# Performance work log

Measured on AMD Instinct MI355X. Metric: run time of the kernel, lower is better.

The kernel has to match this reference:

```python
import jax, jax.numpy as jnp
import numpy as np

N_NODES = 50000
N_EDGES = 800000
D_IN = 128
D_OUT = 64


def setup_inputs() -> dict:
    key = jax.random.key(0)
    k_x, k_src, k_dst, k_val, k_w = jax.random.split(key, 5)
    x = jax.random.normal(k_x, (N_NODES, D_IN), dtype=jnp.float32)
    edge_src = jax.random.randint(k_src, (N_EDGES,), 0, N_NODES, dtype=jnp.int32)
    edge_dst = jnp.sort(jax.random.randint(k_dst, (N_EDGES,), 0, N_NODES, dtype=jnp.int32))
    edge_vals = jax.random.uniform(k_val, (N_EDGES,), dtype=jnp.float32)
    # Xavier-uniform init for weight, zeros for bias (matches reset_parameters)
    limit = float(np.sqrt(6.0 / (D_IN + D_OUT)))
    weight = jax.random.uniform(k_w, (D_IN, D_OUT), minval=-limit, maxval=limit, dtype=jnp.float32)
    bias = jnp.zeros((D_OUT,), dtype=jnp.float32)
    return {"x": x, "edge_src": edge_src, "edge_dst": edge_dst,
            "edge_vals": edge_vals, "weight": weight, "bias": bias}


def reference(x, edge_src, edge_dst, edge_vals, weight, bias):
    # Dense projection: [N, D_in] @ [D_in, D_out] -> [N, D_out]
    h = x @ weight
    # Sparse adjacency matmul (torch.spmm): out[i] = sum_{(j->i) in E} A_val * h[j]
    msgs = edge_vals[:, None] * h[edge_src]          # [E, D_out]
    agg = jax.ops.segment_sum(msgs, edge_dst, num_segments=N_NODES)  # [N, D_out]
    return agg + bias
```

## Files before the change

### kernel.cpp

```cpp
#include <hip/hip_runtime.h>

#define D_IN  128
#define D_OUT 64

typedef float    nfloat4 __attribute__((ext_vector_type(4)));
typedef _Float16 half4_t __attribute__((ext_vector_type(4)));

__global__ __launch_bounds__(256, 4) void gemm_rowptr_kernel(
    const float* __restrict__ x, const float* __restrict__ w,
    _Float16* __restrict__ h, int n_nodes,
    const int* __restrict__ dst, int* __restrict__ row_ptr, int n_edges,
    int gemm_blocks)
{
    __shared__ float Xs[64 * 132];
    __shared__ float Ws[128 * 64];

    if ((int)blockIdx.x >= gemm_blocks) {
        int rb   = (int)blockIdx.x - gemm_blocks;
        int base = rb * 1024 + (int)threadIdx.x;
        #pragma unroll
        for (int j = 0; j < 4; ++j) {
            int e = base + j * 256;
            if (e < n_edges) {
                int d1 = dst[e];
                int d0 = (e == 0) ? -1 : dst[e - 1];
                for (int q = d0 + 1; q <= d1; ++q) row_ptr[q] = e;
                if (e == n_edges - 1) {
                    for (int q = d1 + 1; q <= n_nodes; ++q) row_ptr[q] = n_edges;
                }
            }
        }
        return;
    }

    const int t   = threadIdx.x;
    const int tx  = t & 15;
    const int ty  = t >> 4;
    const int node0 = blockIdx.x * 64;

    #pragma unroll
    for (int j = 0; j < 8; ++j) {
        int idx = j * 256 + t;
        int k   = idx >> 4;
        int c   = idx & 15;
        float4 v = *(const float4*)&w[k * D_OUT + c * 4];
        *(float4*)&Ws[k * 64 + c * 4] = v;
    }
    #pragma unroll
    for (int j = 0; j < 8; ++j) {
        int idx = j * 256 + t;
        int r   = idx >> 5;
        int c   = idx & 31;
        int gn  = node0 + r;
        float4 v = make_float4(0.f, 0.f, 0.f, 0.f);
        if (gn < n_nodes) v = *(const float4*)&x[(size_t)gn * D_IN + c * 4];
        *(float4*)&Xs[r * 132 + c * 4] = v;
    }
    __syncthreads();

    float4 acc[4];
    #pragma unroll
    for (int i = 0; i < 4; ++i) acc[i] = make_float4(0.f, 0.f, 0.f, 0.f);

    const int d0 = tx * 4;
    const int n0 = ty * 4;

    #pragma unroll 2
    for (int k = 0; k < D_IN; k += 4) {
        float4 xa[4], wb[4];
        #pragma unroll
        for (int i = 0; i < 4; ++i)
            xa[i] = *(const float4*)&Xs[(n0 + i) * 132 + k];
        #pragma unroll
        for (int r = 0; r < 4; ++r)
            wb[r] = *(const float4*)&Ws[(k + r) * 64 + d0];
        #pragma unroll
        for (int i = 0; i < 4; ++i) {
            acc[i].x = fmaf(xa[i].x, wb[0].x, acc[i].x);
            acc[i].y = fmaf(xa[i].x, wb[0].y, acc[i].y);
            acc[i].z = fmaf(xa[i].x, wb[0].z, acc[i].z);
            acc[i].w = fmaf(xa[i].x, wb[0].w, acc[i].w);
            acc[i].x = fmaf(xa[i].y, wb[1].x, acc[i].x);
            acc[i].y = fmaf(xa[i].y, wb[1].y, acc[i].y);
            acc[i].z = fmaf(xa[i].y, wb[1].z, acc[i].z);
            acc[i].w = fmaf(xa[i].y, wb[1].w, acc[i].w);
            acc[i].x = fmaf(xa[i].z, wb[2].x, acc[i].x);
            acc[i].y = fmaf(xa[i].z, wb[2].y, acc[i].y);
            acc[i].z = fmaf(xa[i].z, wb[2].z, acc[i].z);
            acc[i].w = fmaf(xa[i].z, wb[2].w, acc[i].w);
            acc[i].x = fmaf(xa[i].w, wb[3].x, acc[i].x);
            acc[i].y = fmaf(xa[i].w, wb[3].y, acc[i].y);
            acc[i].z = fmaf(xa[i].w, wb[3].z, acc[i].z);
            acc[i].w = fmaf(xa[i].w, wb[3].w, acc[i].w);
        }
    }

    #pragma unroll
    for (int i = 0; i < 4; ++i) {
        int gn = node0 + n0 + i;
        if (gn < n_nodes) {
            half4_t hv;
            hv.x = (_Float16)acc[i].x;
            hv.y = (_Float16)acc[i].y;
            hv.z = (_Float16)acc[i].z;
            hv.w = (_Float16)acc[i].w;
            *(half4_t*)&h[(size_t)gn * D_OUT + d0] = hv;
        }
    }
}

__global__ __launch_bounds__(256) void aggregate_kernel(
    const half4_t* __restrict__ h4, const int* __restrict__ src,
    const float* __restrict__ vals, const int* __restrict__ row_ptr,
    const float* __restrict__ bias, float* __restrict__ out, int n_nodes)
{
    int wave = (blockIdx.x * blockDim.x + threadIdx.x) >> 6;
    int lane = threadIdx.x & 63;
    if (wave >= n_nodes) return;
    int sub = lane >> 4;
    int d4  = lane & 15;

    int b = row_ptr[wave];
    int e = row_ptr[wave + 1];

    float4 bb = *(const float4*)&bias[d4 * 4];

    float4 acc0 = make_float4(0.f, 0.f, 0.f, 0.f);
    float4 acc1 = make_float4(0.f, 0.f, 0.f, 0.f);

    int k = b + sub;
    for (; k + 12 < e; k += 16) {
        int   s0 = __builtin_nontemporal_load(&src[k]);
        int   s1 = __builtin_nontemporal_load(&src[k + 4]);
        int   s2 = __builtin_nontemporal_load(&src[k + 8]);
        int   s3 = __builtin_nontemporal_load(&src[k + 12]);
        float v0 = __builtin_nontemporal_load(&vals[k]);
        float v1 = __builtin_nontemporal_load(&vals[k + 4]);
        float v2 = __builtin_nontemporal_load(&vals[k + 8]);
        float v3 = __builtin_nontemporal_load(&vals[k + 12]);
        half4_t h0 = h4[(size_t)s0 * 16 + d4];
        half4_t h1 = h4[(size_t)s1 * 16 + d4];
        half4_t h2 = h4[(size_t)s2 * 16 + d4];
        half4_t h3 = h4[(size_t)s3 * 16 + d4];
        acc0.x = fmaf(v0, (float)h0.x, acc0.x);
        acc0.y = fmaf(v0, (float)h0.y, acc0.y);
        acc0.z = fmaf(v0, (float)h0.z, acc0.z);
        acc0.w = fmaf(v0, (float)h0.w, acc0.w);
        acc1.x = fmaf(v1, (float)h1.x, acc1.x);
        acc1.y = fmaf(v1, (float)h1.y, acc1.y);
        acc1.z = fmaf(v1, (float)h1.z, acc1.z);
        acc1.w = fmaf(v1, (float)h1.w, acc1.w);
        acc0.x = fmaf(v2, (float)h2.x, acc0.x);
        acc0.y = fmaf(v2, (float)h2.y, acc0.y);
        acc0.z = fmaf(v2, (float)h2.z, acc0.z);
        acc0.w = fmaf(v2, (float)h2.w, acc0.w);
        acc1.x = fmaf(v3, (float)h3.x, acc1.x);
        acc1.y = fmaf(v3, (float)h3.y, acc1.y);
        acc1.z = fmaf(v3, (float)h3.z, acc1.z);
        acc1.w = fmaf(v3, (float)h3.w, acc1.w);
    }
    for (; k + 4 < e; k += 8) {
        int   s0 = __builtin_nontemporal_load(&src[k]);
        int   s1 = __builtin_nontemporal_load(&src[k + 4]);
        float v0 = __builtin_nontemporal_load(&vals[k]);
        float v1 = __builtin_nontemporal_load(&vals[k + 4]);
        half4_t h0 = h4[(size_t)s0 * 16 + d4];
        half4_t h1 = h4[(size_t)s1 * 16 + d4];
        acc0.x = fmaf(v0, (float)h0.x, acc0.x);
        acc0.y = fmaf(v0, (float)h0.y, acc0.y);
        acc0.z = fmaf(v0, (float)h0.z, acc0.z);
        acc0.w = fmaf(v0, (float)h0.w, acc0.w);
        acc1.x = fmaf(v1, (float)h1.x, acc1.x);
        acc1.y = fmaf(v1, (float)h1.y, acc1.y);
        acc1.z = fmaf(v1, (float)h1.z, acc1.z);
        acc1.w = fmaf(v1, (float)h1.w, acc1.w);
    }
    if (k < e) {
        int   s0 = src[k];
        float v0 = vals[k];
        half4_t h0 = h4[(size_t)s0 * 16 + d4];
        acc0.x = fmaf(v0, (float)h0.x, acc0.x);
        acc0.y = fmaf(v0, (float)h0.y, acc0.y);
        acc0.z = fmaf(v0, (float)h0.z, acc0.z);
        acc0.w = fmaf(v0, (float)h0.w, acc0.w);
    }

    float4 acc;
    acc.x = acc0.x + acc1.x;
    acc.y = acc0.y + acc1.y;
    acc.z = acc0.z + acc1.z;
    acc.w = acc0.w + acc1.w;

    #pragma unroll
    for (int off = 16; off < 64; off <<= 1) {
        acc.x += __shfl_xor(acc.x, off, 64);
        acc.y += __shfl_xor(acc.y, off, 64);
        acc.z += __shfl_xor(acc.z, off, 64);
        acc.w += __shfl_xor(acc.w, off, 64);
    }

    if (sub == 0) {
        nfloat4 o;
        o.x = acc.x + bb.x;
        o.y = acc.y + bb.y;
        o.z = acc.z + bb.z;
        o.w = acc.w + bb.w;
        __builtin_nontemporal_store(o, (nfloat4*)&out[(size_t)wave * D_OUT + d4 * 4]);
    }
}

extern "C" void kernel_launch(void* const* d_in, const int* in_sizes, int n_in,
                              void* d_out, int out_size, void* d_ws, size_t ws_size,
                              hipStream_t stream)
{
    const float* x         = (const float*)d_in[0];
    const int*   edge_src  = (const int*)  d_in[1];
    const int*   edge_dst  = (const int*)  d_in[2];
    const float* edge_vals = (const float*)d_in[3];
    const float* weight    = (const float*)d_in[4];
    const float* bias      = (const float*)d_in[5];
    float*       out       = (float*)d_out;

    const int n_nodes = in_sizes[0] / D_IN;
    const int n_edges = in_sizes[1];

    _Float16* h       = (_Float16*)d_ws;
    int*      row_ptr = (int*)((char*)d_ws + (size_t)n_nodes * D_OUT * sizeof(_Float16));

    {
        int gemm_blocks = (n_nodes + 63) / 64;
        int rp_blocks   = (n_edges + 1023) / 1024;
        dim3 grid(gemm_blocks + rp_blocks), block(256);
        hipLaunchKernelGGL(gemm_rowptr_kernel, grid, block, 0, stream,
                           x, weight, h, n_nodes,
                           edge_dst, row_ptr, n_edges, gemm_blocks);
    }
    {
        dim3 grid((n_nodes + 3) / 4), block(256);
        hipLaunchKernelGGL(aggregate_kernel, grid, block, 0, stream,
                           (const half4_t*)h, edge_src, edge_vals, row_ptr, bias, out, n_nodes);
    }
}
```

Baseline: 124.3 us.

## Fuse GEMM, row-pointer build and aggregation into one cooperative persistent kernel

Merges the projection/row_ptr kernel and the aggregation kernel into a single cooperative launch. Blocks loop persistently over GEMM and row_ptr work units, meet at a grid-wide sync, then walk nodes with a grid-stride loop to aggregate. The X tile is no longer staged in shared memory; each thread reads x straight from global memory with clamped row indices. This removes the second kernel launch and the gap between kernels, but adds a grid barrier, limits how many blocks can be resident at once, and loses the shared-memory reuse of x.

```diff
diff --git a/kernel.cpp b/kernel.cpp
--- a/kernel.cpp
+++ b/kernel.cpp
@@ -1,4 +1,7 @@
 #include <hip/hip_runtime.h>
+#include <hip/hip_cooperative_groups.h>
+
+namespace cg = cooperative_groups;
 
 #define D_IN  128
 #define D_OUT 64
@@ -6,206 +9,204 @@
 typedef float    nfloat4 __attribute__((ext_vector_type(4)));
 typedef _Float16 half4_t __attribute__((ext_vector_type(4)));
 
-__global__ __launch_bounds__(256, 4) void gemm_rowptr_kernel(
+__global__ __launch_bounds__(256, 4) void fused_gcn_kernel(
     const float* __restrict__ x, const float* __restrict__ w,
     _Float16* __restrict__ h, int n_nodes,
     const int* __restrict__ dst, int* __restrict__ row_ptr, int n_edges,
-    int gemm_blocks)
+    const int* __restrict__ src, const float* __restrict__ vals,
+    const float* __restrict__ bias, float* __restrict__ out,
+    int gemm_units, int total_units)
 {
-    __shared__ float Xs[64 * 132];
     __shared__ float Ws[128 * 64];
 
-    if ((int)blockIdx.x >= gemm_blocks) {
-        int rb   = (int)blockIdx.x - gemm_blocks;
-        int base = rb * 1024 + (int)threadIdx.x;
-        #pragma unroll
-        for (int j = 0; j < 4; ++j) {
-            int e = base + j * 256;
-            if (e < n_edges) {
-                int d1 = dst[e];
-                int d0 = (e == 0) ? -1 : dst[e - 1];
-                for (int q = d0 + 1; q <= d1; ++q) row_ptr[q] = e;
-                if (e == n_edges - 1) {
-                    for (int q = d1 + 1; q <= n_nodes; ++q) row_ptr[q] = n_edges;
-                }
-            }
-        }
-        return;
-    }
-
-    const int t   = threadIdx.x;
-    const int tx  = t & 15;
-    const int ty  = t >> 4;
-    const int node0 = blockIdx.x * 64;
+    const int t = threadIdx.x;
 
     #pragma unroll
     for (int j = 0; j < 8; ++j) {
         int idx = j * 256 + t;
         int k   = idx >> 4;
         int c   = idx & 15;
-        float4 v = *(const float4*)&w[k * D_OUT + c * 4];
-        *(float4*)&Ws[k * 64 + c * 4] = v;
-    }
-    #pragma unroll
-    for (int j = 0; j < 8; ++j) {
-        int idx = j * 256 + t;
-        int r   = idx >> 5;
-        int c   = idx & 31;
-        int gn  = node0 + r;
-        float4 v = make_float4(0.f, 0.f, 0.f, 0.f);
-        if (gn < n_nodes) v = *(const float4*)&x[(size_t)gn * D_IN + c * 4];
-        *(float4*)&Xs[r * 132 + c * 4] = v;
+        *(float4*)&Ws[k * 64 + c * 4] = *(const float4*)&w[k * D_OUT + c * 4];
     }
     __syncthreads();
 
-    float4 acc[4];
-    #pragma unroll
-    for (int i = 0; i < 4; ++i) acc[i] = make_float4(0.f, 0.f, 0.f, 0.f);
-
+    const int tx = t & 15;
+    const int ty = t >> 4;
     const int d0 = tx * 4;
     const int n0 = ty * 4;
 
-    #pragma unroll 2
-    for (int k = 0; k < D_IN; k += 4) {
-        float4 xa[4], wb[4];
+    for (int u = blockIdx.x; u < total_units; u += gridDim.x) {
+        if (u < gemm_units) {
+            const int node0 = u * 64;
+            const int r0    = node0 + n0;
+            int ri[4];
+            #pragma unroll
+            for (int i = 0; i < 4; ++i) {
+                int g = r0 + i;
+                ri[i] = (g < n_nodes) ? g : (n_nodes - 1);
+            }
+
+            float4 acc[4];
+            #pragma unroll
+            for (int i = 0; i < 4; ++i) acc[i] = make_float4(0.f, 0.f, 0.f, 0.f);
+
+            #pragma unroll 2
+            for (int k = 0; k < D_IN; k += 4) {
+                float4 xa[4], wb[4];
+                #pragma unroll
+                for (int i = 0; i < 4; ++i)
+                    xa[i] = *(const float4*)&x[(size_t)ri[i] * D_IN + k];
+                #pragma unroll
+                for (int r = 0; r < 4; ++r)
+                    wb[r] = *(const float4*)&Ws[(k + r) * 64 + d0];
+                #pragma unroll
+                for (int i = 0; i < 4; ++i) {
+                    acc[i].x = fmaf(xa[i].x, wb[0].x, acc[i].x);
+                    acc[i].y = fmaf(xa[i].x, wb[0].y, acc[i].y);
+                    acc[i].z = fmaf(xa[i].x, wb[0].z, acc[i].z);
+                    acc[i].w = fmaf(xa[i].x, wb[0].w, acc[i].w);
+                    acc[i].x = fmaf(xa[i].y, wb[1].x, acc[i].x);
+                    acc[i].y = fmaf(xa[i].y, wb[1].y, acc[i].y);
+                    acc[i].z = fmaf(xa[i].y, wb[1].z, acc[i].z);
+                    acc[i].w = fmaf(xa[i].y, wb[1].w, acc[i].w);
+                    acc[i].x = fmaf(xa[i].z, wb[2].x, acc[i].x);
+                    acc[i].y = fmaf(xa[i].z, wb[2].y, acc[i].y);
+                    acc[i].z = fmaf(xa[i].z, wb[2].z, acc[i].z);
+                    acc[i].w = fmaf(xa[i].z, wb[2].w, acc[i].w);
+                    acc[i].x = fmaf(xa[i].w, wb[3].x, acc[i].x);
+                    acc[i].y = fmaf(xa[i].w, wb[3].y, acc[i].y);
+                    acc[i].z = fmaf(xa[i].w, wb[3].z, acc[i].z);
+                    acc[i].w = fmaf(xa[i].w, wb[3].w, acc[i].w);
+                }
+            }
+
+            #pragma unroll
+            for (int i = 0; i < 4; ++i) {
+                int gn = r0 + i;
+                if (gn < n_nodes) {
+                    half4_t hv;
+                    hv.x = (_Float16)acc[i].x;
+                    hv.y = (_Float16)acc[i].y;
+                    hv.z = (_Float16)acc[i].z;
+                    hv.w = (_Float16)acc[i].w;
+                    *(half4_t*)&h[(size_t)gn * D_OUT + d0] = hv;
+                }
+            }
+        } else {
+            int rb   = u - gemm_units;
+            int base = rb * 1024 + t;
+            #pragma unroll
+            for (int j = 0; j < 4; ++j) {
+                int e = base + j * 256;
+                if (e < n_edges) {
+                    int d1 = dst[e];
+                    int dp = (e == 0) ? -1 : dst[e - 1];
+                    for (int q = dp + 1; q <= d1; ++q) row_ptr[q] = e;
+                    if (e == n_edges - 1) {
+                        for (int q = d1 + 1; q <= n_nodes; ++q) row_ptr[q] = n_edges;
+                    }
+                }
+            }
+        }
+    }
+
+    cg::this_grid().sync();
+
+    const int lane = t & 63;
+    const int sub  = lane >> 4;
+    const int d4   = lane & 15;
+    const int wv   = (int)((blockIdx.x * blockDim.x + t) >> 6);
+    const int nwv  = (int)((gridDim.x * blockDim.x) >> 6);
+    const half4_t* __restrict__ h4 = (const half4_t*)h;
+
+    float4 bb = *(const float4*)&bias[d4 * 4];
+
+    for (int node = wv; node < n_nodes; node += nwv) {
+        int b = row_ptr[node];
+        int e = row_ptr[node + 1];
+
+        float4 acc0 = make_float4(0.f, 0.f, 0.f, 0.f);
+        float4 acc1 = make_float4(0.f, 0.f, 0.f, 0.f);
+
+        int k = b + sub;
+        for (; k + 12 < e; k += 16) {
+            int   s0 = __builtin_nontemporal_load(&src[k]);
+            int   s1 = __builtin_nontemporal_load(&src[k + 4]);
+            int   s2 = __builtin_nontemporal_load(&src[k + 8]);
+            int   s3 = __builtin_nontemporal_load(&src[k + 12]);
+            float v0 = __builtin_nontemporal_load(&vals[k]);
+            float v1 = __builtin_nontemporal_load(&vals[k + 4]);
+            float v2 = __builtin_nontemporal_load(&vals[k + 8]);
+            float v3 = __builtin_nontemporal_load(&vals[k + 12]);
+            half4_t h0 = h4[(size_t)s0 * 16 + d4];
+            half4_t h1 = h4[(size_t)s1 * 16 + d4];
+            half4_t h2 = h4[(size_t)s2 * 16 + d4];
+            half4_t h3 = h4[(size_t)s3 * 16 + d4];
+            acc0.x = fmaf(v0, (float)h0.x, acc0.x);
+            acc0.y = fmaf(v0, (float)h0.y, acc0.y);
+            acc0.z = fmaf(v0, (float)h0.z, acc0.z);
+            acc0.w = fmaf(v0, (float)h0.w, acc0.w);
+            acc1.x = fmaf(v1, (float)h1.x, acc1.x);
+            acc1.y = fmaf(v1, (float)h1.y, acc1.y);
+            acc1.z = fmaf(v1, (float)h1.z, acc1.z);
+            acc1.w = fmaf(v1, (float)h1.w, acc1.w);
+            acc0.x = fmaf(v2, (float)h2.x, acc0.x);
+            acc0.y = fmaf(v2, (float)h2.y, acc0.y);
+            acc0.z = fmaf(v2, (float)h2.z, acc0.z);
+            acc0.w = fmaf(v2, (float)h2.w, acc0.w);
+            acc1.x = fmaf(v3, (float)h3.x, acc1.x);
+            acc1.y = fmaf(v3, (float)h3.y, acc1.y);
+            acc1.z = fmaf(v3, (float)h3.z, acc1.z);
+            acc1.w = fmaf(v3, (float)h3.w, acc1.w);
+        }
+        for (; k + 4 < e; k += 8) {
+            int   s0 = __builtin_nontemporal_load(&src[k]);
+            int   s1 = __builtin_nontemporal_load(&src[k + 4]);
+            float v0 = __builtin_nontemporal_load(&vals[k]);
+            float v1 = __builtin_nontemporal_load(&vals[k + 4]);
+            half4_t h0 = h4[(size_t)s0 * 16 + d4];
+            half4_t h1 = h4[(size_t)s1 * 16 + d4];
+            acc0.x = fmaf(v0, (float)h0.x, acc0.x);
+            acc0.y = fmaf(v0, (float)h0.y, acc0.y);
+            acc0.z = fmaf(v0, (float)h0.z, acc0.z);
+            acc0.w = fmaf(v0, (float)h0.w, acc0.w);
+            acc1.x = fmaf(v1, (float)h1.x, acc1.x);
+            acc1.y = fmaf(v1, (float)h1.y, acc1.y);
+            acc1.z = fmaf(v1, (float)h1.z, acc1.z);
+            acc1.w = fmaf(v1, (float)h1.w, acc1.w);
+        }
+        if (k < e) {
+            int   s0 = src[k];
+            float v0 = vals[k];
+            half4_t h0 = h4[(size_t)s0 * 16 + d4];
+            acc0.x = fmaf(v0, (float)h0.x, acc0.x);
+            acc0.y = fmaf(v0, (float)h0.y, acc0.y);
+            acc0.z = fmaf(v0, (float)h0.z, acc0.z);
+            acc0.w = fmaf(v0, (float)h0.w, acc0.w);
+        }
+
+        float4 acc;
+        acc.x = acc0.x + acc1.x;
+        acc.y = acc0.y + acc1.y;
+        acc.z = acc0.z + acc1.z;
+        acc.w = acc0.w + acc1.w;
+
         #pragma unroll
-        for (int i = 0; i < 4; ++i)
-            xa[i] = *(const float4*)&Xs[(n0 + i) * 132 + k];
-        #pragma unroll
-        for (int r = 0; r < 4; ++r)
-            wb[r] = *(const float4*)&Ws[(k + r) * 64 + d0];
-        #pragma unroll
-        for (int i = 0; i < 4; ++i) {
-            acc[i].x = fmaf(xa[i].x, wb[0].x, acc[i].x);
-            acc[i].y = fmaf(xa[i].x, wb[0].y, acc[i].y);
-            acc[i].z = fmaf(xa[i].x, wb[0].z, acc[i].z);
-            acc[i].w = fmaf(xa[i].x, wb[0].w, acc[i].w);
-            acc[i].x = fmaf(xa[i].y, wb[1].x, acc[i].x);
-            acc[i].y = fmaf(xa[i].y, wb[1].y, acc[i].y);
-            acc[i].z = fmaf(xa[i].y, wb[1].z, acc[i].z);
-            acc[i].w = fmaf(xa[i].y, wb[1].w, acc[i].w);
-            acc[i].x = fmaf(xa[i].z, wb[2].x, acc[i].x);
-            acc[i].y = fmaf(xa[i].z, wb[2].y, acc[i].y);
-            acc[i].z = fmaf(xa[i].z, wb[2].z, acc[i].z);
-            acc[i].w = fmaf(xa[i].z, wb[2].w, acc[i].w);
-            acc[i].x = fmaf(xa[i].w, wb[3].x, acc[i].x);
-            acc[i].y = fmaf(xa[i].w, wb[3].y, acc[i].y);
-            acc[i].z = fmaf(xa[i].w, wb[3].z, acc[i].z);
-            acc[i].w = fmaf(xa[i].w, wb[3].w, acc[i].w);
-        }
-    }
-
-    #pragma unroll
-    for (int i = 0; i < 4; ++i) {
-        int gn = node0 + n0 + i;
-        if (gn < n_nodes) {
-            half4_t hv;
-            hv.x = (_Float16)acc[i].x;
-            hv.y = (_Float16)acc[i].y;
-            hv.z = (_Float16)acc[i].z;
-            hv.w = (_Float16)acc[i].w;
-            *(half4_t*)&h[(size_t)gn * D_OUT + d0] = hv;
-        }
-    }
-}
-
-__global__ __launch_bounds__(256) void aggregate_kernel(
-    const half4_t* __restrict__ h4, const int* __restrict__ src,
-    const float* __restrict__ vals, const int* __restrict__ row_ptr,
-    const float* __restrict__ bias, float* __restrict__ out, int n_nodes)
-{
-    int wave = (blockIdx.x * blockDim.x + threadIdx.x) >> 6;
-    int lane = threadIdx.x & 63;
-    if (wave >= n_nodes) return;
-    int sub = lane >> 4;
-    int d4  = lane & 15;
-
-    int b = row_ptr[wave];
-    int e = row_ptr[wave + 1];
-
-    float4 bb = *(const float4*)&bias[d4 * 4];
-
-    float4 acc0 = make_float4(0.f, 0.f, 0.f, 0.f);
-    float4 acc1 = make_float4(0.f, 0.f, 0.f, 0.f);
-
-    int k = b + sub;
-    for (; k + 12 < e; k += 16) {
-        int   s0 = __builtin_nontemporal_load(&src[k]);
-        int   s1 = __builtin_nontemporal_load(&src[k + 4]);
-        int   s2 = __builtin_nontemporal_load(&src[k + 8]);
-        int   s3 = __builtin_nontemporal_load(&src[k + 12]);
-        float v0 = __builtin_nontemporal_load(&vals[k]);
-        float v1 = __builtin_nontemporal_load(&vals[k + 4]);
-        float v2 = __builtin_nontemporal_load(&vals[k + 8]);
-        float v3 = __builtin_nontemporal_load(&vals[k + 12]);
-        half4_t h0 = h4[(size_t)s0 * 16 + d4];
-        half4_t h1 = h4[(size_t)s1 * 16 + d4];
-        half4_t h2 = h4[(size_t)s2 * 16 + d4];
-        half4_t h3 = h4[(size_t)s3 * 16 + d4];
-        acc0.x = fmaf(v0, (float)h0.x, acc0.x);
-        acc0.y = fmaf(v0, (float)h0.y, acc0.y);
-        acc0.z = fmaf(v0, (float)h0.z, acc0.z);
-        acc0.w = fmaf(v0, (float)h0.w, acc0.w);
-        acc1.x = fmaf(v1, (float)h1.x, acc1.x);
-        acc1.y = fmaf(v1, (float)h1.y, acc1.y);
-        acc1.z = fmaf(v1, (float)h1.z, acc1.z);
-        acc1.w = fmaf(v1, (float)h1.w, acc1.w);
-        acc0.x = fmaf(v2, (float)h2.x, acc0.x);
-        acc0.y = fmaf(v2, (float)h2.y, acc0.y);
-        acc0.z = fmaf(v2, (float)h2.z, acc0.z);
-        acc0.w = fmaf(v2, (float)h2.w, acc0.w);
-        acc1.x = fmaf(v3, (float)h3.x, acc1.x);
-        acc1.y = fmaf(v3, (float)h3.y, acc1.y);
-        acc1.z = fmaf(v3, (float)h3.z, acc1.z);
-        acc1.w = fmaf(v3, (float)h3.w, acc1.w);
-    }
-    for (; k + 4 < e; k += 8) {
-        int   s0 = __builtin_nontemporal_load(&src[k]);
-        int   s1 = __builtin_nontemporal_load(&src[k + 4]);
-        float v0 = __builtin_nontemporal_load(&vals[k]);
-        float v1 = __builtin_nontemporal_load(&vals[k + 4]);
-        half4_t h0 = h4[(size_t)s0 * 16 + d4];
-        half4_t h1 = h4[(size_t)s1 * 16 + d4];
-        acc0.x = fmaf(v0, (float)h0.x, acc0.x);
-        acc0.y = fmaf(v0, (float)h0.y, acc0.y);
-        acc0.z = fmaf(v0, (float)h0.z, acc0.z);
-        acc0.w = fmaf(v0, (float)h0.w, acc0.w);
-        acc1.x = fmaf(v1, (float)h1.x, acc1.x);
-        acc1.y = fmaf(v1, (float)h1.y, acc1.y);
-        acc1.z = fmaf(v1, (float)h1.z, acc1.z);
-        acc1.w = fmaf(v1, (float)h1.w, acc1.w);
-    }
-    if (k < e) {
-        int   s0 = src[k];
-        float v0 = vals[k];
-        half4_t h0 = h4[(size_t)s0 * 16 + d4];
-        acc0.x = fmaf(v0, (float)h0.x, acc0.x);
-        acc0.y = fmaf(v0, (float)h0.y, acc0.y);
-        acc0.z = fmaf(v0, (float)h0.z, acc0.z);
-        acc0.w = fmaf(v0, (float)h0.w, acc0.w);
-    }
-
-    float4 acc;
-    acc.x = acc0.x + acc1.x;
-    acc.y = acc0.y + acc1.y;
-    acc.z = acc0.z + acc1.z;
-    acc.w = acc0.w + acc1.w;
-
-    #pragma unroll
-    for (int off = 16; off < 64; off <<= 1) {
-        acc.x += __shfl_xor(acc.x, off, 64);
-        acc.y += __shfl_xor(acc.y, off, 64);
-        acc.z += __shfl_xor(acc.z, off, 64);
-        acc.w += __shfl_xor(acc.w, off, 64);
-    }
-
-    if (sub == 0) {
-        nfloat4 o;
-        o.x = acc.x + bb.x;
-        o.y = acc.y + bb.y;
-        o.z = acc.z + bb.z;
-        o.w = acc.w + bb.w;
-        __builtin_nontemporal_store(o, (nfloat4*)&out[(size_t)wave * D_OUT + d4 * 4]);
+        for (int off = 16; off < 64; off <<= 1) {
+            acc.x += __shfl_xor(acc.x, off, 64);
+            acc.y += __shfl_xor(acc.y, off, 64);
+            acc.z += __shfl_xor(acc.z, off, 64);
+            acc.w += __shfl_xor(acc.w, off, 64);
+        }
+
+        if (sub == 0) {
+            nfloat4 o;
+            o.x = acc.x + bb.x;
+            o.y = acc.y + bb.y;
+            o.z = acc.z + bb.z;
+            o.w = acc.w + bb.w;
+            __builtin_nontemporal_store(o, (nfloat4*)&out[(size_t)node * D_OUT + d4 * 4]);
+        }
     }
 }
 
@@ -227,17 +228,31 @@
     _Float16* h       = (_Float16*)d_ws;
     int*      row_ptr = (int*)((char*)d_ws + (size_t)n_nodes * D_OUT * sizeof(_Float16));
 
-    {
-        int gemm_blocks = (n_nodes + 63) / 64;
-        int rp_blocks   = (n_edges + 1023) / 1024;
-        dim3 grid(gemm_blocks + rp_blocks), block(256);
-        hipLaunchKernelGGL(gemm_rowptr_kernel, grid, block, 0, stream,
-                           x, weight, h, n_nodes,
-                           edge_dst, row_ptr, n_edges, gemm_blocks);
-    }
-    {
-        dim3 grid((n_nodes + 3) / 4), block(256);
-        hipLaunchKernelGGL(aggregate_kernel, grid, block, 0, stream,
-                           (const half4_t*)h, edge_src, edge_vals, row_ptr, bias, out, n_nodes);
-    }
+    static int grid_blocks = 0;
+    if (grid_blocks == 0) {
+        int dev = 0;
+        (void)hipGetDevice(&dev);
+        int ncu = 256;
+        (void)hipDeviceGetAttribute(&ncu, hipDeviceAttributeMultiprocessorCount, dev);
+        int maxb = 0;
+        if (hipOccupancyMaxActiveBlocksPerMultiprocessor(&maxb, fused_gcn_kernel, 256, 0)
+                != hipSuccess || maxb < 1)
+            maxb = 2;
+        grid_blocks = ncu * maxb;
+        if (grid_blocks < 64) grid_blocks = 64;
+    }
+
+    int gemm_units  = (n_nodes + 63) / 64;
+    int rp_units    = (n_edges + 1023) / 1024;
+    int total_units = gemm_units + rp_units;
+
+    void* args[] = {
+        (void*)&x, (void*)&weight, (void*)&h, (void*)&n_nodes,
+        (void*)&edge_dst, (void*)&row_ptr, (void*)&n_edges,
+        (void*)&edge_src, (void*)&edge_vals,
+        (void*)&bias, (void*)&out,
+        (void*)&gemm_units, (void*)&total_units
+    };
+    hipLaunchCooperativeKernel((const void*)fused_gcn_kernel,
+                               dim3(grid_blocks), dim3(256), args, 0, stream);
 }
```

Result: slower. 221.0 us (+77.9%).
